# Performance work log

Measured on AMD Instinct MI355X. Metric: run time of the kernel, lower is better.

The kernel has to match this reference:

```python
import jax, jax.numpy as jnp
import numpy as np

B, L, H = 4, 2048, 1024
NH = 16
DK = H // NH


def setup_inputs() -> dict:
    key = jax.random.key(0)
    ks = jax.random.split(key, 9)
    s = 1.0 / np.sqrt(H)
    return {
        "x": jax.random.normal(ks[0], (B, L, H), dtype=jnp.float32),
        "Wq": jax.random.uniform(ks[1], (H, H), jnp.float32, -s, s),
        "bq": jnp.zeros((H,), jnp.float32),
        "Wk": jax.random.uniform(ks[2], (H, H), jnp.float32, -s, s),
        "bk": jnp.zeros((H,), jnp.float32),
        "Wv": jax.random.uniform(ks[3], (H, H), jnp.float32, -s, s),
        "bv": jnp.zeros((H,), jnp.float32),
        "Wo": jax.random.uniform(ks[4], (H, H), jnp.float32, -s, s),
        "bo": jnp.zeros((H,), jnp.float32),
    }


def reference(x, Wq, bq, Wk, bk, Wv, bv, Wo, bo):
    # Linear projections (torch Linear: x @ W.T + b), split heads -> (B, NH, L, DK)
    def proj(W, b):
        y = jnp.einsum("blh,oh->blo", x, W) + b
        return y.reshape(B, L, NH, DK).transpose(0, 2, 1, 3)

    q = proj(Wq, bq)
    k = proj(Wk, bk)
    v = proj(Wv, bv)

    scale = jnp.sqrt(jnp.asarray(DK, x.dtype))
    scores = jnp.einsum("bnqd,bnkd->bnqk", q, k) / scale  # (B, NH, L, L)
    attn = jax.nn.softmax(scores, axis=-1)
    # dropout is identity in eval mode
    context = jnp.einsum("bnqk,bnkd->bnqd", attn, v)
    context = context.transpose(0, 2, 1, 3).reshape(B, L, H)
    out = jnp.einsum("blh,oh->blo", context, Wo) + bo

    pooled = out.mean(axis=1)                 # (B, H)
    weights = attn.mean(axis=1).mean(axis=1)  # (B, L)
    return pooled, weights
```

## Files before the change

### kernel.cpp

```cpp
#include <hip/hip_runtime.h>
#include <math.h>

#define B_  4
#define L_  2048
#define H_  1024
#define NH_ 16
#define DK_ 64

#define QSC 0.18033688011112043f

typedef unsigned short ushort_t;
typedef __attribute__((ext_vector_type(8))) short short8;
typedef __attribute__((ext_vector_type(4))) float f32x4;

__device__ __forceinline__ ushort_t f2b(float f) {
    unsigned int u = __float_as_uint(f);
    return (ushort_t)((u + 0x7FFFu + ((u >> 16) & 1u)) >> 16);
}
__device__ __forceinline__ float b2f(ushort_t h) {
    return __uint_as_float(((unsigned int)h) << 16);
}
__device__ __forceinline__ float fexp2(float x) {
    return __builtin_amdgcn_exp2f(x);
}

__device__ __forceinline__ void gload_lds16(const void* g, void* l) {
    __builtin_amdgcn_global_load_lds((const __attribute__((address_space(1))) void*)g,
                                     (__attribute__((address_space(3))) void*)l, 16, 0, 0);
}

__global__ __launch_bounds__(256) void fsplit_kernel(const float* __restrict__ src,
                                                     ushort_t* __restrict__ ph,
                                                     ushort_t* __restrict__ pl, int n4)
{
    int i = blockIdx.x * 256 + threadIdx.x;
    if (i < n4) {
        float4 v = ((const float4*)src)[i];
        ushort4 h, l;
        float f[4] = {v.x, v.y, v.z, v.w};
        ushort_t hh[4], ll[4];
        #pragma unroll
        for (int e = 0; e < 4; ++e) {
            hh[e] = f2b(f[e]);
            ll[e] = f2b(f[e] - b2f(hh[e]));
        }
        h.x = hh[0]; h.y = hh[1]; h.z = hh[2]; h.w = hh[3];
        l.x = ll[0]; l.y = ll[1]; l.z = ll[2]; l.w = ll[3];
        ((ushort4*)ph)[i] = h;
        ((ushort4*)pl)[i] = l;
    }
}

__global__ __launch_bounds__(256) void proj_split(
    const ushort_t* __restrict__ xh, const ushort_t* __restrict__ xl,
    const ushort_t* __restrict__ Wqh,
    const ushort_t* __restrict__ Wkh, const ushort_t* __restrict__ Wkl,
    const float* __restrict__ bq, const float* __restrict__ bk,
    ushort_t* __restrict__ qho,
    ushort_t* __restrict__ kho, ushort_t* __restrict__ klo)
{
    const int z = blockIdx.z;
    const ushort_t* Wh = z ? Wkh : Wqh;
    const ushort_t* Wl = Wkl;
    const float* bias  = z ? bk  : bq;

    const int n0 = blockIdx.y * 128;
    const int o0 = blockIdx.x * 128;

    __shared__ ushort_t Ash[128 * 32];
    __shared__ ushort_t Asl[128 * 32];
    __shared__ ushort_t Bsh[128 * 32];
    __shared__ ushort_t Bsl[128 * 32];

    const int t = threadIdx.x;
    const int lane = t & 63, w = t >> 6;
    const int ln = lane & 15, qd = lane >> 4;
    const int wy = w >> 1, wx = w & 1;
    const int ldsbase = (t & ~63) * 8;

    int rowS[2], cS[2];
    #pragma unroll
    for (int i = 0; i < 2; ++i) {
        int slot = i * 256 + t;
        rowS[i] = slot >> 2;
        cS[i] = (slot & 3) ^ ((rowS[i] >> 1) & 3);
    }

    f32x4 acc[4][4];
    #pragma unroll
    for (int i = 0; i < 4; ++i)
        #pragma unroll
        for (int j = 0; j < 4; ++j) acc[i][j] = (f32x4){0.f, 0.f, 0.f, 0.f};

    for (int k0 = 0; k0 < H_; k0 += 32) {
        __syncthreads();
        #pragma unroll
        for (int i = 0; i < 2; ++i) {
            gload_lds16(xh + (size_t)(n0 + rowS[i]) * H_ + k0 + cS[i] * 8,
                        &Ash[i * 2048 + ldsbase]);
            gload_lds16(xl + (size_t)(n0 + rowS[i]) * H_ + k0 + cS[i] * 8,
                        &Asl[i * 2048 + ldsbase]);
            gload_lds16(Wh + (size_t)(o0 + rowS[i]) * H_ + k0 + cS[i] * 8,
                        &Bsh[i * 2048 + ldsbase]);
        }
        if (z) {
            #pragma unroll
            for (int i = 0; i < 2; ++i)
                gload_lds16(Wl + (size_t)(o0 + rowS[i]) * H_ + k0 + cS[i] * 8,
                            &Bsl[i * 2048 + ldsbase]);
        }
        __syncthreads();

        short8 bh4[4], bl4[4];
        #pragma unroll
        for (int nt = 0; nt < 4; ++nt) {
            int row = wx * 64 + nt * 16 + ln;
            int sz = (qd ^ ((row >> 1) & 3)) << 3;
            bh4[nt] = *(const short8*)&Bsh[row * 32 + sz];
            if (z) bl4[nt] = *(const short8*)&Bsl[row * 32 + sz];
        }
        #pragma unroll
        for (int mt = 0; mt < 4; ++mt) {
            int row = wy * 64 + mt * 16 + ln;
            int sz = (qd ^ ((row >> 1) & 3)) << 3;
            short8 ah = *(const short8*)&Ash[row * 32 + sz];
            short8 al = *(const short8*)&Asl[row * 32 + sz];
            if (z) {
                #pragma unroll
                for (int nt = 0; nt < 4; ++nt) {
                    acc[mt][nt] = __builtin_amdgcn_mfma_f32_16x16x32_bf16(al, bh4[nt], acc[mt][nt], 0, 0, 0);
                    acc[mt][nt] = __builtin_amdgcn_mfma_f32_16x16x32_bf16(ah, bl4[nt], acc[mt][nt], 0, 0, 0);
                    acc[mt][nt] = __builtin_amdgcn_mfma_f32_16x16x32_bf16(ah, bh4[nt], acc[mt][nt], 0, 0, 0);
                }
            } else {
                #pragma unroll
                for (int nt = 0; nt < 4; ++nt) {
                    acc[mt][nt] = __builtin_amdgcn_mfma_f32_16x16x32_bf16(al, bh4[nt], acc[mt][nt], 0, 0, 0);
                    acc[mt][nt] = __builtin_amdgcn_mfma_f32_16x16x32_bf16(ah, bh4[nt], acc[mt][nt], 0, 0, 0);
                }
            }
        }
    }

    #pragma unroll
    for (int nt = 0; nt < 4; ++nt) {
        int o = o0 + wx * 64 + nt * 16 + ln;
        float bvv = bias[o];
        int hh = o >> 6, d = o & 63;
        #pragma unroll
        for (int mt = 0; mt < 4; ++mt) {
            #pragma unroll
            for (int r = 0; r < 4; ++r) {
                int n = n0 + wy * 64 + mt * 16 + qd * 4 + r;
                int bb = n >> 11, l = n & (L_ - 1);
                size_t idx = (((size_t)(bb * NH_ + hh) * L_ + l) << 6) + d;
                float val = acc[mt][nt][r] + bvv;
                if (z) {
                    ushort_t vh = f2b(val);
                    kho[idx] = vh;
                    klo[idx] = f2b(val - b2f(vh));
                } else {
                    qho[idx] = f2b(val * QSC);
                }
            }
        }
    }
}

__global__ __launch_bounds__(256) void attn_split(
    const ushort_t* __restrict__ qh,
    const ushort_t* __restrict__ kh, const ushort_t* __restrict__ kl,
    float* __restrict__ cs)
{
    const int qt = blockIdx.x & 15;
    const int bh = blockIdx.x >> 4;

    const int t = threadIdx.x;
    const int lane = t & 63, w = t >> 6;
    const int ln = lane & 15, qd = lane >> 4;

    __shared__ ushort_t Ksh[64 * 64];
    __shared__ ushort_t Ksl[64 * 64];
    __shared__ float cs_all[4][64];

    const size_t headoff = (size_t)bh * L_ * DK_;
    const size_t qoff0 = headoff + ((size_t)(qt * 128 + w * 32 + ln)) * DK_;
    const size_t qoff1 = qoff0 + 16 * DK_;
    short8 aqh[2][2];
    aqh[0][0] = *(const short8*)(qh + qoff0 + qd * 8);
    aqh[0][1] = *(const short8*)(qh + qoff0 + 32 + qd * 8);
    aqh[1][0] = *(const short8*)(qh + qoff1 + qd * 8);
    aqh[1][1] = *(const short8*)(qh + qoff1 + 32 + qd * 8);

    int rowS[2], cS[2];
    #pragma unroll
    for (int i = 0; i < 2; ++i) {
        int slot = i * 256 + t;
        rowS[i] = slot >> 3;
        cS[i] = (slot & 7) ^ (rowS[i] & 7);
    }

    float l_run[2][4] = {};

    for (int kt = 0; kt < 32; ++kt) {
        __syncthreads();
        #pragma unroll
        for (int i = 0; i < 2; ++i)
            gload_lds16(kh + headoff + ((size_t)(kt * 64 + rowS[i]) << 6) + cS[i] * 8,
                        &Ksh[i * 2048 + (t & ~63) * 8]);
        __syncthreads();

        #pragma unroll
        for (int nt = 0; nt < 4; ++nt) {
            int kr = nt * 16 + ln;
            int sz0 = ((qd     ^ (kr & 7)) << 3);
            int sz1 = (((qd + 4) ^ (kr & 7)) << 3);
            short8 b0h = *(const short8*)&Ksh[kr * 64 + sz0];
            short8 b1h = *(const short8*)&Ksh[kr * 64 + sz1];
            #pragma unroll
            for (int s = 0; s < 2; ++s) {
                f32x4 zz = (f32x4){0.f, 0.f, 0.f, 0.f};
                zz = __builtin_amdgcn_mfma_f32_16x16x32_bf16(aqh[s][0], b0h, zz, 0, 0, 0);
                zz = __builtin_amdgcn_mfma_f32_16x16x32_bf16(aqh[s][1], b1h, zz, 0, 0, 0);
                #pragma unroll
                for (int r = 0; r < 4; ++r)
                    l_run[s][r] += fexp2(zz[r]);
            }
        }
    }

    #pragma unroll
    for (int off = 1; off < 16; off <<= 1)
        #pragma unroll
        for (int s = 0; s < 2; ++s)
            #pragma unroll
            for (int r = 0; r < 4; ++r)
                l_run[s][r] += __shfl_xor(l_run[s][r], off);
    float inv_l[2][4];
    #pragma unroll
    for (int s = 0; s < 2; ++s)
        #pragma unroll
        for (int r = 0; r < 4; ++r) inv_l[s][r] = 1.0f / l_run[s][r];

    for (int kt = 0; kt < 32; ++kt) {
        __syncthreads();
        #pragma unroll
        for (int i = 0; i < 2; ++i) {
            gload_lds16(kh + headoff + ((size_t)(kt * 64 + rowS[i]) << 6) + cS[i] * 8,
                        &Ksh[i * 2048 + (t & ~63) * 8]);
            gload_lds16(kl + headoff + ((size_t)(kt * 64 + rowS[i]) << 6) + cS[i] * 8,
                        &Ksl[i * 2048 + (t & ~63) * 8]);
        }
        __syncthreads();

        float colp[4];
        #pragma unroll
        for (int nt = 0; nt < 4; ++nt) {
            int kr = nt * 16 + ln;
            int sz0 = ((qd     ^ (kr & 7)) << 3);
            int sz1 = (((qd + 4) ^ (kr & 7)) << 3);
            short8 b0h = *(const short8*)&Ksh[kr * 64 + sz0];
            short8 b1h = *(const short8*)&Ksh[kr * 64 + sz1];
            short8 b0l = *(const short8*)&Ksl[kr * 64 + sz0];
            short8 b1l = *(const short8*)&Ksl[kr * 64 + sz1];
            float cp = 0.f;
            #pragma unroll
            for (int s = 0; s < 2; ++s) {
                f32x4 zz = (f32x4){0.f, 0.f, 0.f, 0.f};
                zz = __builtin_amdgcn_mfma_f32_16x16x32_bf16(aqh[s][0], b0l, zz, 0, 0, 0);
                zz = __builtin_amdgcn_mfma_f32_16x16x32_bf16(aqh[s][1], b1l, zz, 0, 0, 0);
                zz = __builtin_amdgcn_mfma_f32_16x16x32_bf16(aqh[s][0], b0h, zz, 0, 0, 0);
                zz = __builtin_amdgcn_mfma_f32_16x16x32_bf16(aqh[s][1], b1h, zz, 0, 0, 0);
                cp += fexp2(zz[0]) * inv_l[s][0] + fexp2(zz[1]) * inv_l[s][1]
                    + fexp2(zz[2]) * inv_l[s][2] + fexp2(zz[3]) * inv_l[s][3];
            }
            colp[nt] = cp;
        }
        #pragma unroll
        for (int nt = 0; nt < 4; ++nt) {
            colp[nt] += __shfl_xor(colp[nt], 16);
            colp[nt] += __shfl_xor(colp[nt], 32);
        }
        float mine = (qd == 0) ? colp[0] : (qd == 1) ? colp[1] : (qd == 2) ? colp[2] : colp[3];
        cs_all[w][lane] = mine;
        __syncthreads();
        if (t < 64) {
            float tot = cs_all[0][t] + cs_all[1][t] + cs_all[2][t] + cs_all[3][t];
            atomicAdd(&cs[(size_t)bh * L_ + kt * 64 + t], tot);
        }
    }
}

__global__ __launch_bounds__(256) void ctx1_kernel(
    const float* __restrict__ cs, const float* __restrict__ x, float* __restrict__ T)
{
    const int o0 = blockIdx.x * 64, b = blockIdx.y, l0 = blockIdx.z * 256;
    const int t = threadIdx.x, o = t & 63, hg = t >> 6;
    __shared__ float cs_s[16][128];
    float acc[4] = {};

    for (int ch = 0; ch < 2; ++ch) {
        int lbase = l0 + ch * 128;
        __syncthreads();
        for (int i = t; i < 2048; i += 256) {
            int h = i >> 7, lc = i & 127;
            cs_s[h][lc] = cs[((size_t)(b * NH_ + h) << 11) + lbase + lc];
        }
        __syncthreads();
        for (int lc = 0; lc < 128; ++lc) {
            float xv = x[((size_t)(b * L_ + lbase + lc) << 10) + o0 + o];
            #pragma unroll
            for (int j = 0; j < 4; ++j) acc[j] += cs_s[hg * 4 + j][lc] * xv;
        }
    }
    #pragma unroll
    for (int j = 0; j < 4; ++j)
        atomicAdd(&T[((size_t)(b * NH_ + hg * 4 + j) << 10) + o0 + o], acc[j]);
}

__global__ __launch_bounds__(256) void ctx2_kernel(
    const float* __restrict__ T, const float* __restrict__ Wv,
    const float* __restrict__ bv, float* __restrict__ ctx)
{
    const int gid  = blockIdx.x * 4 + (threadIdx.x >> 6);
    const int lane = threadIdx.x & 63;
    const int b = gid >> 10, o = gid & (H_ - 1);
    const float4* wr = (const float4*)(Wv + (size_t)o * H_);
    const float4* tr = (const float4*)(T + ((size_t)(b * NH_ + (o >> 6)) << 10));
    float acc = 0.f;
    #pragma unroll
    for (int i = 0; i < 4; ++i) {
        float4 wv = wr[lane + i * 64];
        float4 tv = tr[lane + i * 64];
        acc += wv.x * tv.x + wv.y * tv.y + wv.z * tv.z + wv.w * tv.w;
    }
    #pragma unroll
    for (int off = 32; off; off >>= 1) acc += __shfl_xor(acc, off);
    if (lane == 0) ctx[(b << 10) + o] = acc + (float)L_ * bv[o];
}

__global__ __launch_bounds__(256) void pooled_kernel(
    const float* __restrict__ ctx, const float* __restrict__ Wo,
    const float* __restrict__ bo, float* __restrict__ out)
{
    const int gid  = blockIdx.x * 4 + (threadIdx.x >> 6);
    const int lane = threadIdx.x & 63;
    const int b = gid >> 10, o = gid & (H_ - 1);
    const float4* wr = (const float4*)(Wo + (size_t)o * H_);
    const float4* cr = (const float4*)(ctx + ((size_t)b << 10));
    float acc = 0.f;
    #pragma unroll
    for (int i = 0; i < 4; ++i) {
        float4 wv = wr[lane + i * 64];
        float4 cv = cr[lane + i * 64];
        acc += wv.x * cv.x + wv.y * cv.y + wv.z * cv.z + wv.w * cv.w;
    }
    #pragma unroll
    for (int off = 32; off; off >>= 1) acc += __shfl_xor(acc, off);
    if (lane == 0) out[(b << 10) + o] = acc * (1.0f / (float)L_) + bo[o];
}

__global__ void weights_kernel(const float* __restrict__ cs, float* __restrict__ out)
{
    int i = blockIdx.x * 256 + threadIdx.x;
    int b = i >> 11, k = i & (L_ - 1);
    float s = 0.f;
    #pragma unroll
    for (int h = 0; h < NH_; ++h) s += cs[((size_t)(b * NH_ + h) << 11) + k];
    out[B_ * H_ + i] = s * (1.0f / (float)(NH_ * L_));
}

extern "C" void kernel_launch(void* const* d_in, const int* in_sizes, int n_in,
                              void* d_out, int out_size, void* d_ws, size_t ws_size,
                              hipStream_t stream)
{
    const float* x  = (const float*)d_in[0];
    const float* Wq = (const float*)d_in[1];
    const float* bq = (const float*)d_in[2];
    const float* Wk = (const float*)d_in[3];
    const float* bk = (const float*)d_in[4];
    const float* Wv = (const float*)d_in[5];
    const float* bv = (const float*)d_in[6];
    const float* Wo = (const float*)d_in[7];
    const float* bo = (const float*)d_in[8];
    float* out = (float*)d_out;

    float* ws  = (float*)d_ws;
    float* cs  = ws;
    float* T   = ws + 131072;
    float* ctx = ws + 196608;
    ushort_t* base = (ushort_t*)(ws + 200704);
    const size_t QE = 8388608;
    ushort_t* qhb = base;
    ushort_t* khb = base + QE;
    ushort_t* klb = base + 2 * QE;
    ushort_t* xhb = base + 3 * QE;
    ushort_t* xlb = base + 4 * QE;
    ushort_t* wqh = base + 5 * QE;
    ushort_t* wql = wqh + 1048576;
    ushort_t* wkh = wql + 1048576;
    ushort_t* wkl = wkh + 1048576;

    hipMemsetAsync(ws, 0, (131072 + 65536) * sizeof(float), stream);

    fsplit_kernel<<<8192, 256, 0, stream>>>(x,  xhb, xlb, 2097152);
    fsplit_kernel<<<1024, 256, 0, stream>>>(Wq, wqh, wql, 262144);
    fsplit_kernel<<<1024, 256, 0, stream>>>(Wk, wkh, wkl, 262144);

    proj_split<<<dim3(8, 64, 2), 256, 0, stream>>>(xhb, xlb, wqh, wkh, wkl,
                                                   bq, bk, qhb, khb, klb);

    attn_split<<<B_ * NH_ * (L_ / 128), 256, 0, stream>>>(qhb, khb, klb, cs);

    ctx1_kernel<<<dim3(16, 4, 8), 256, 0, stream>>>(cs, x, T);
    ctx2_kernel<<<1024, 256, 0, stream>>>(T, Wv, bv, ctx);
    pooled_kernel<<<1024, 256, 0, stream>>>(ctx, Wo, bo, out);
    weights_kernel<<<(B_ * L_) / 256, 256, 0, stream>>>(cs, out);
}
```

Baseline: 366.0 us.

## Double-buffer K tiles in attention, fuse split launches, use per-wave atomics

The attention kernel now double-buffers the K-high and K-low LDS tiles. It prefetches tile kt+1 while computing on tile kt, needs only one barrier per iteration, and starts the second pass's first tile load before the softmax-denominator reduction. The cross-wave LDS reduction of column sums is removed: each wave issues its own atomicAdd, which cuts a barrier per iteration at the cost of four times as many global atomics. The three float-to-bf16 hi/lo split launches are merged into one kernel so two launches disappear. LDS use doubles, which may reduce occupancy.

```diff
diff --git a/kernel.cpp b/kernel.cpp
--- a/kernel.cpp
+++ b/kernel.cpp
@@ -29,26 +29,30 @@
                                      (__attribute__((address_space(3))) void*)l, 16, 0, 0);
 }
 
-__global__ __launch_bounds__(256) void fsplit_kernel(const float* __restrict__ src,
-                                                     ushort_t* __restrict__ ph,
-                                                     ushort_t* __restrict__ pl, int n4)
-{
-    int i = blockIdx.x * 256 + threadIdx.x;
-    if (i < n4) {
-        float4 v = ((const float4*)src)[i];
-        ushort4 h, l;
-        float f[4] = {v.x, v.y, v.z, v.w};
-        ushort_t hh[4], ll[4];
-        #pragma unroll
-        for (int e = 0; e < 4; ++e) {
-            hh[e] = f2b(f[e]);
-            ll[e] = f2b(f[e] - b2f(hh[e]));
-        }
-        h.x = hh[0]; h.y = hh[1]; h.z = hh[2]; h.w = hh[3];
-        l.x = ll[0]; l.y = ll[1]; l.z = ll[2]; l.w = ll[3];
-        ((ushort4*)ph)[i] = h;
-        ((ushort4*)pl)[i] = l;
-    }
+__global__ __launch_bounds__(256) void fsplit3_kernel(
+    const float* __restrict__ x, const float* __restrict__ Wq, const float* __restrict__ Wk,
+    ushort_t* __restrict__ xh, ushort_t* __restrict__ xl,
+    ushort_t* __restrict__ wqh, ushort_t* __restrict__ wql,
+    ushort_t* __restrict__ wkh, ushort_t* __restrict__ wkl)
+{
+    int bid = blockIdx.x;
+    const float* src; ushort_t *ph, *pl; int i;
+    if (bid < 8192)      { src = x;  ph = xh;  pl = xl;  i = bid * 256 + threadIdx.x; }
+    else if (bid < 9216) { src = Wq; ph = wqh; pl = wql; i = (bid - 8192) * 256 + threadIdx.x; }
+    else                 { src = Wk; ph = wkh; pl = wkl; i = (bid - 9216) * 256 + threadIdx.x; }
+    float4 v = ((const float4*)src)[i];
+    float f[4] = {v.x, v.y, v.z, v.w};
+    ushort4 h, l;
+    ushort_t hh[4], ll[4];
+    #pragma unroll
+    for (int e = 0; e < 4; ++e) {
+        hh[e] = f2b(f[e]);
+        ll[e] = f2b(f[e] - b2f(hh[e]));
+    }
+    h.x = hh[0]; h.y = hh[1]; h.z = hh[2]; h.w = hh[3];
+    l.x = ll[0]; l.y = ll[1]; l.z = ll[2]; l.w = ll[3];
+    ((ushort4*)ph)[i] = h;
+    ((ushort4*)pl)[i] = l;
 }
 
 __global__ __launch_bounds__(256) void proj_split(
@@ -179,9 +183,8 @@
     const int lane = t & 63, w = t >> 6;
     const int ln = lane & 15, qd = lane >> 4;
 
-    __shared__ ushort_t Ksh[64 * 64];
-    __shared__ ushort_t Ksl[64 * 64];
-    __shared__ float cs_all[4][64];
+    __shared__ ushort_t Ksh[2][64 * 64];
+    __shared__ ushort_t Ksl[2][64 * 64];
 
     const size_t headoff = (size_t)bh * L_ * DK_;
     const size_t qoff0 = headoff + ((size_t)(qt * 128 + w * 32 + ln)) * DK_;
@@ -199,70 +202,94 @@
         rowS[i] = slot >> 3;
         cS[i] = (slot & 7) ^ (rowS[i] & 7);
     }
+    const int ldsb = (t & ~63) * 8;
+    const ushort_t* pkh[2];
+    const ushort_t* pkl[2];
+    #pragma unroll
+    for (int i = 0; i < 2; ++i) {
+        pkh[i] = kh + headoff + ((size_t)rowS[i] << 6) + cS[i] * 8;
+        pkl[i] = kl + headoff + ((size_t)rowS[i] << 6) + cS[i] * 8;
+    }
 
     float l_run[2][4] = {};
 
+    {
+        const ushort_t* ph[2] = {pkh[0], pkh[1]};
+        #pragma unroll
+        for (int i = 0; i < 2; ++i)
+            gload_lds16(ph[i], &Ksh[0][i * 2048 + ldsb]);
+
+        for (int kt = 0; kt < 32; ++kt) {
+            const int cb = kt & 1;
+            __syncthreads();
+            if (kt + 1 < 32) {
+                #pragma unroll
+                for (int i = 0; i < 2; ++i)
+                    gload_lds16(ph[i] + (size_t)(kt + 1) * 4096,
+                                &Ksh[cb ^ 1][i * 2048 + ldsb]);
+            }
+            #pragma unroll
+            for (int nt = 0; nt < 4; ++nt) {
+                int kr = nt * 16 + ln;
+                int sz0 = ((qd     ^ (kr & 7)) << 3);
+                int sz1 = (((qd + 4) ^ (kr & 7)) << 3);
+                short8 b0h = *(const short8*)&Ksh[cb][kr * 64 + sz0];
+                short8 b1h = *(const short8*)&Ksh[cb][kr * 64 + sz1];
+                #pragma unroll
+                for (int s = 0; s < 2; ++s) {
+                    f32x4 zz = (f32x4){0.f, 0.f, 0.f, 0.f};
+                    zz = __builtin_amdgcn_mfma_f32_16x16x32_bf16(aqh[s][0], b0h, zz, 0, 0, 0);
+                    zz = __builtin_amdgcn_mfma_f32_16x16x32_bf16(aqh[s][1], b1h, zz, 0, 0, 0);
+                    #pragma unroll
+                    for (int r = 0; r < 4; ++r)
+                        l_run[s][r] += fexp2(zz[r]);
+                }
+            }
+        }
+    }
+
+    #pragma unroll
+    for (int i = 0; i < 2; ++i) {
+        gload_lds16(pkh[i], &Ksh[0][i * 2048 + ldsb]);
+        gload_lds16(pkl[i], &Ksl[0][i * 2048 + ldsb]);
+    }
+
+    #pragma unroll
+    for (int off = 1; off < 16; off <<= 1)
+        #pragma unroll
+        for (int s = 0; s < 2; ++s)
+            #pragma unroll
+            for (int r = 0; r < 4; ++r)
+                l_run[s][r] += __shfl_xor(l_run[s][r], off);
+    float inv_l[2][4];
+    #pragma unroll
+    for (int s = 0; s < 2; ++s)
+        #pragma unroll
+        for (int r = 0; r < 4; ++r) inv_l[s][r] = 1.0f / l_run[s][r];
+
     for (int kt = 0; kt < 32; ++kt) {
+        const int cb = kt & 1;
         __syncthreads();
-        #pragma unroll
-        for (int i = 0; i < 2; ++i)
-            gload_lds16(kh + headoff + ((size_t)(kt * 64 + rowS[i]) << 6) + cS[i] * 8,
-                        &Ksh[i * 2048 + (t & ~63) * 8]);
-        __syncthreads();
-
+        if (kt + 1 < 32) {
+            #pragma unroll
+            for (int i = 0; i < 2; ++i) {
+                gload_lds16(pkh[i] + (size_t)(kt + 1) * 4096,
+                            &Ksh[cb ^ 1][i * 2048 + ldsb]);
+                gload_lds16(pkl[i] + (size_t)(kt + 1) * 4096,
+                            &Ksl[cb ^ 1][i * 2048 + ldsb]);
+            }
+        }
+
+        float colp[4];
         #pragma unroll
         for (int nt = 0; nt < 4; ++nt) {
             int kr = nt * 16 + ln;
             int sz0 = ((qd     ^ (kr & 7)) << 3);
             int sz1 = (((qd + 4) ^ (kr & 7)) << 3);
-            short8 b0h = *(const short8*)&Ksh[kr * 64 + sz0];
-            short8 b1h = *(const short8*)&Ksh[kr * 64 + sz1];
-            #pragma unroll
-            for (int s = 0; s < 2; ++s) {
-                f32x4 zz = (f32x4){0.f, 0.f, 0.f, 0.f};
-                zz = __builtin_amdgcn_mfma_f32_16x16x32_bf16(aqh[s][0], b0h, zz, 0, 0, 0);
-                zz = __builtin_amdgcn_mfma_f32_16x16x32_bf16(aqh[s][1], b1h, zz, 0, 0, 0);
-                #pragma unroll
-                for (int r = 0; r < 4; ++r)
-                    l_run[s][r] += fexp2(zz[r]);
-            }
-        }
-    }
-
-    #pragma unroll
-    for (int off = 1; off < 16; off <<= 1)
-        #pragma unroll
-        for (int s = 0; s < 2; ++s)
-            #pragma unroll
-            for (int r = 0; r < 4; ++r)
-                l_run[s][r] += __shfl_xor(l_run[s][r], off);
-    float inv_l[2][4];
-    #pragma unroll
-    for (int s = 0; s < 2; ++s)
-        #pragma unroll
-        for (int r = 0; r < 4; ++r) inv_l[s][r] = 1.0f / l_run[s][r];
-
-    for (int kt = 0; kt < 32; ++kt) {
-        __syncthreads();
-        #pragma unroll
-        for (int i = 0; i < 2; ++i) {
-            gload_lds16(kh + headoff + ((size_t)(kt * 64 + rowS[i]) << 6) + cS[i] * 8,
-                        &Ksh[i * 2048 + (t & ~63) * 8]);
-            gload_lds16(kl + headoff + ((size_t)(kt * 64 + rowS[i]) << 6) + cS[i] * 8,
-                        &Ksl[i * 2048 + (t & ~63) * 8]);
-        }
-        __syncthreads();
-
-        float colp[4];
-        #pragma unroll
-        for (int nt = 0; nt < 4; ++nt) {
-            int kr = nt * 16 + ln;
-            int sz0 = ((qd     ^ (kr & 7)) << 3);
-            int sz1 = (((qd + 4) ^ (kr & 7)) << 3);
-            short8 b0h = *(const short8*)&Ksh[kr * 64 + sz0];
-            short8 b1h = *(const short8*)&Ksh[kr * 64 + sz1];
-            short8 b0l = *(const short8*)&Ksl[kr * 64 + sz0];
-            short8 b1l = *(const short8*)&Ksl[kr * 64 + sz1];
+            short8 b0h = *(const short8*)&Ksh[cb][kr * 64 + sz0];
+            short8 b1h = *(const short8*)&Ksh[cb][kr * 64 + sz1];
+            short8 b0l = *(const short8*)&Ksl[cb][kr * 64 + sz0];
+            short8 b1l = *(const short8*)&Ksl[cb][kr * 64 + sz1];
             float cp = 0.f;
             #pragma unroll
             for (int s = 0; s < 2; ++s) {
@@ -282,12 +309,7 @@
             colp[nt] += __shfl_xor(colp[nt], 32);
         }
         float mine = (qd == 0) ? colp[0] : (qd == 1) ? colp[1] : (qd == 2) ? colp[2] : colp[3];
-        cs_all[w][lane] = mine;
-        __syncthreads();
-        if (t < 64) {
-            float tot = cs_all[0][t] + cs_all[1][t] + cs_all[2][t] + cs_all[3][t];
-            atomicAdd(&cs[(size_t)bh * L_ + kt * 64 + t], tot);
-        }
+        atomicAdd(&cs[(size_t)bh * L_ + kt * 64 + lane], mine);
     }
 }
 
@@ -403,9 +425,8 @@
 
     hipMemsetAsync(ws, 0, (131072 + 65536) * sizeof(float), stream);
 
-    fsplit_kernel<<<8192, 256, 0, stream>>>(x,  xhb, xlb, 2097152);
-    fsplit_kernel<<<1024, 256, 0, stream>>>(Wq, wqh, wql, 262144);
-    fsplit_kernel<<<1024, 256, 0, stream>>>(Wk, wkh, wkl, 262144);
+    fsplit3_kernel<<<10240, 256, 0, stream>>>(x, Wq, Wk, xhb, xlb,
+                                              wqh, wql, wkh, wkl);
 
     proj_split<<<dim3(8, 64, 2), 256, 0, stream>>>(xhb, xlb, wqh, wkh, wkl,
                                                    bq, bk, qhb, khb, klb);
```

New measurement: 381.4 us. 1.04x slower.
